# Optimization experiments

Hardware: AMD Instinct MI355X
Metric: run time of the kernel (lower is better)

Reference implementation:

```python
import jax, jax.numpy as jnp
import numpy as np

N_EMBD = 1024
N_HEAD = 16
HEAD_DIM = N_EMBD // N_HEAD


def setup_inputs() -> dict:
    key = jax.random.key(0)
    ks = jax.random.split(key, 6)
    B, T, C = 4, 2048, N_EMBD
    scale = 1.0 / np.sqrt(C)
    x = jax.random.normal(ks[0], (B, T, C), dtype=jnp.float32)
    Wq = jax.random.normal(ks[1], (C, C), dtype=jnp.float32) * scale
    Wk = jax.random.normal(ks[2], (C, C), dtype=jnp.float32) * scale
    Wv = jax.random.normal(ks[3], (C, C), dtype=jnp.float32) * scale
    Wo = jax.random.normal(ks[4], (C, C), dtype=jnp.float32) * scale
    bo = jax.random.normal(ks[5], (C,), dtype=jnp.float32) * 0.01
    return {"x": x, "Wq": Wq, "Wk": Wk, "Wv": Wv, "Wo": Wo, "bo": bo}


def reference(x, Wq, Wk, Wv, Wo, bo):
    B, T, C = x.shape
    H, D = N_HEAD, HEAD_DIM
    # projections (torch Linear: x @ W.T); reshape to [B, H, T, D]
    q = (x @ Wq.T).reshape(B, T, H, D).transpose(0, 2, 1, 3)
    k = (x @ Wk.T).reshape(B, T, H, D).transpose(0, 2, 1, 3)
    v = (x @ Wv.T).reshape(B, T, H, D).transpose(0, 2, 1, 3)
    scores = jnp.einsum("bhqd,bhkd->bhqk", q, k) / np.sqrt(D)
    causal = jnp.tril(jnp.ones((T, T), dtype=bool))  # True = keep
    scores = jnp.where(causal, scores, -jnp.inf)
    attn = jax.nn.softmax(scores, axis=-1)
    # dropout in eval mode = identity
    out = jnp.einsum("bhqk,bhkd->bhqd", attn, v)
    out = out.transpose(0, 2, 1, 3).reshape(B, T, C)
    return out @ Wo.T + bo
```

## Files before the change

### kernel.cpp

```cpp
#include <hip/hip_runtime.h>

typedef __attribute__((ext_vector_type(4))) float floatx4;
typedef __attribute__((ext_vector_type(8))) __bf16 bf16x8;
typedef __attribute__((ext_vector_type(8))) unsigned short ushort8;
typedef __attribute__((ext_vector_type(4))) unsigned short ushort4v;

#define MFMA16(a, b, c) __builtin_amdgcn_mfma_f32_16x16x32_bf16((a), (b), (c), 0, 0, 0)

static __device__ __forceinline__ unsigned short f2bu(float f) {
  unsigned int u = __builtin_bit_cast(unsigned int, f);
  unsigned int r = (u + 0x7fffu + ((u >> 16) & 1u)) >> 16;
  return (unsigned short)r;
}

static __device__ __forceinline__ unsigned int cvtpk(float lo, float hi) {
  unsigned int r;
  asm("v_cvt_pk_bf16_f32 %0, %1, %2" : "=v"(r) : "v"(lo), "v"(hi));
  return r;
}

static __device__ __forceinline__ float fexp2(float x) {
  float r;
  asm("v_exp_f32 %0, %1" : "=v"(r) : "v"(x));
  return r;
}

static __device__ __forceinline__ void gload_lds16(const void* g, void* l) {
  __builtin_amdgcn_global_load_lds((const __attribute__((address_space(1))) void*)g,
                                   (__attribute__((address_space(3))) void*)l, 16, 0, 0);
}

__global__ void cast_all(const float* __restrict__ x,  unsigned short* __restrict__ xb,
                         const float* __restrict__ w0, unsigned short* __restrict__ w0b,
                         const float* __restrict__ w1, unsigned short* __restrict__ w1b,
                         const float* __restrict__ w2, unsigned short* __restrict__ w2b,
                         const float* __restrict__ w3, unsigned short* __restrict__ w3b) {
  int i = blockIdx.x * blockDim.x + threadIdx.x;
  const float* src;
  unsigned short* dst;
  int j;
  if (i < 2097152) {
    src = x; dst = xb; j = i;
  } else {
    j = i - 2097152;
    int wsel = j >> 18;
    j &= 262143;
    src = (wsel == 0) ? w0 : (wsel == 1) ? w1 : (wsel == 2) ? w2 : w3;
    dst = (wsel == 0) ? w0b : (wsel == 1) ? w1b : (wsel == 2) ? w2b : w3b;
  }
  float4 v = reinterpret_cast<const float4*>(src)[j];
  ushort4v o;
  o.x = f2bu(v.x); o.y = f2bu(v.y); o.z = f2bu(v.z); o.w = f2bu(v.w);
  reinterpret_cast<ushort4v*>(dst)[j] = o;
}

static __device__ __forceinline__ void gemm_core(const unsigned short* __restrict__ Ag,
                                                 const unsigned short* __restrict__ Wg,
                                                 int tm0, int tn0,
                                                 unsigned short* As, unsigned short* Bs,
                                                 floatx4 acc[4][4]) {
  const int tid = threadIdx.x;
  const int w = tid >> 6, l = tid & 63;
  const int lg = l >> 4, lq = l & 15;
  const int wr = w >> 1, wc = w & 1;

  const int srow = w * 32 + (l >> 2);
  const int scol = (l & 3) * 8;
  const unsigned short* ga = Ag + (size_t)(tm0 + srow) * 1024 + scol;
  const unsigned short* gb = Wg + (size_t)(tn0 + srow) * 1024 + scol;
  const int ldst0 = w * 1024;
  const int ldst1 = ldst0 + 16 * 32;

#define GSTAGE(bi, kt_)                                   \
  do {                                                    \
    const int ko_ = (kt_) * 32;                           \
    gload_lds16(ga + ko_,              As + (bi) * 4096 + ldst0); \
    gload_lds16(ga + ko_ + 16 * 1024,  As + (bi) * 4096 + ldst1); \
    gload_lds16(gb + ko_,              Bs + (bi) * 4096 + ldst0); \
    gload_lds16(gb + ko_ + 16 * 1024,  Bs + (bi) * 4096 + ldst1); \
  } while (0)

  GSTAGE(0, 0);
  __syncthreads();
  int buf = 0;
  for (int kt = 0; kt < 32; ++kt) {
    if (kt + 1 < 32) GSTAGE(buf ^ 1, kt + 1);
    bf16x8 ar[4], br[4];
#pragma unroll
    for (int i = 0; i < 4; ++i) {
      ar[i] = *(const bf16x8*)(As + buf * 4096 + (wr * 64 + i * 16 + lq) * 32 + lg * 8);
      br[i] = *(const bf16x8*)(Bs + buf * 4096 + (wc * 64 + i * 16 + lq) * 32 + lg * 8);
    }
#pragma unroll
    for (int i = 0; i < 4; ++i)
#pragma unroll
      for (int j = 0; j < 4; ++j)
        acc[i][j] = MFMA16(ar[i], br[j], acc[i][j]);
    __syncthreads();
    buf ^= 1;
  }
#undef GSTAGE
}

__global__ __launch_bounds__(256, 4) void gemm_qkv(const unsigned short* __restrict__ xb,
                                                   const unsigned short* __restrict__ Wqb,
                                                   const unsigned short* __restrict__ Wkb,
                                                   const unsigned short* __restrict__ Wvb,
                                                   unsigned short* __restrict__ Qb,
                                                   unsigned short* __restrict__ Kb,
                                                   unsigned short* __restrict__ Vtb) {
  __shared__ unsigned short As[2 * 128 * 32];
  __shared__ unsigned short Bs[2 * 128 * 32];
  const int tid = threadIdx.x;
  const int w = tid >> 6, l = tid & 63;
  const int lg = l >> 4, lq = l & 15;
  const int wr = w >> 1, wc = w & 1;
  const int tm0 = blockIdx.x * 128;
  const int tn0 = blockIdx.y * 128;
  const int z = blockIdx.z;
  const unsigned short* W = (z == 0) ? Wqb : (z == 1) ? Wkb : Wvb;

  floatx4 acc[4][4];
#pragma unroll
  for (int i = 0; i < 4; ++i)
#pragma unroll
    for (int j = 0; j < 4; ++j) acc[i][j] = (floatx4){0.f, 0.f, 0.f, 0.f};

  gemm_core(xb, W, tm0, tn0, As, Bs, acc);

  const int b = tm0 >> 11;
  const int t0 = tm0 & 2047;

  if (z == 2) {
#pragma unroll
    for (int mi = 0; mi < 4; ++mi)
#pragma unroll
      for (int ni = 0; ni < 4; ++ni) {
        int t = t0 + wr * 64 + mi * 16 + lg * 4;
        int n = tn0 + wc * 64 + ni * 16 + lq;
        int h = n >> 6, d = n & 63;
        ushort4v o;
        o.x = f2bu(acc[mi][ni][0]);
        o.y = f2bu(acc[mi][ni][1]);
        o.z = f2bu(acc[mi][ni][2]);
        o.w = f2bu(acc[mi][ni][3]);
        *(ushort4v*)(Vtb + ((size_t)(b * 16 + h) * 64 + d) * 2048 + t) = o;
      }
  } else {
    float sc = (z == 0) ? 0.125f * 1.44269504f : 1.0f;
    unsigned short* dst = (z == 0) ? Qb : Kb;
#pragma unroll
    for (int mi = 0; mi < 4; ++mi)
#pragma unroll
      for (int ni = 0; ni < 4; ++ni) {
        int n = tn0 + wc * 64 + ni * 16 + lq;
        int h = n >> 6, d = n & 63;
#pragma unroll
        for (int r = 0; r < 4; ++r) {
          int t = t0 + wr * 64 + mi * 16 + lg * 4 + r;
          dst[((size_t)(b * 16 + h) * 2048 + t) * 64 + d] = f2bu(acc[mi][ni][r] * sc);
        }
      }
  }
}

__global__ __launch_bounds__(256) void attn_fwd(const unsigned short* __restrict__ Qb,
                                                const unsigned short* __restrict__ Kb,
                                                const unsigned short* __restrict__ Vtb,
                                                unsigned short* __restrict__ attb) {
  constexpr int T = 2048;
  __shared__ char Ls[32768];
  const int bh = blockIdx.x;
  const int pr = blockIdx.y;
  const int tid = threadIdx.x;
  const int w = tid >> 6, l = tid & 63;
  const int lg = l >> 4, lq = l & 15;

  const char* Kgc = (const char*)(Kb + (size_t)bh * T * 64);
  const char* Vgc = (const char*)(Vtb + (size_t)bh * 64 * T);
  const unsigned short* Qp = Qb + (size_t)bh * T * 64;

  const int scolx = ((tid & 7) << 4) ^ (((tid >> 3) & 7) << 4);
  const int koff = ((tid >> 3) << 7) + scolx;
  const int voff = ((tid >> 3) << 12) + scolx;
  char* Ks = (char*)Ls;
  char* Vs = (char*)Ls + 16384;
  const int kswz = (lq & 7) << 4;
  const int wofs = w * 1024;
  const int b = bh >> 4, h = bh & 15;

  const ushort8 onesu = {0x3F80, 0x3F80, 0x3F80, 0x3F80, 0x3F80, 0x3F80, 0x3F80, 0x3F80};
  const bf16x8 onesf = __builtin_bit_cast(bf16x8, onesu);

#define STAGE(bi, kb_)                                               \
  do {                                                               \
    const char* kg_ = Kgc + (size_t)(kb_) * 128 + koff;              \
    const char* vg_ = Vgc + (size_t)(kb_) * 2 + voff;                \
    gload_lds16(kg_,          Ks + (bi) * 8192 + wofs);              \
    gload_lds16(kg_ + 4096,   Ks + (bi) * 8192 + 4096 + wofs);       \
    gload_lds16(vg_,          Vs + (bi) * 8192 + wofs);              \
    gload_lds16(vg_ + 131072, Vs + (bi) * 8192 + 4096 + wofs);       \
  } while (0)

  for (int pi = 0; pi < 2; ++pi) {
    const int qt = pi ? (31 - pr) : pr;
    const int q0 = qt * 64 + w * 16;
    const int qrow = q0 + lq;

    bf16x8 qf0 = *(const bf16x8*)(Qp + (size_t)qrow * 64 + lg * 8);
    bf16x8 qf1 = *(const bf16x8*)(Qp + (size_t)qrow * 64 + 32 + lg * 8);

    floatx4 acc[4];
#pragma unroll
    for (int dc = 0; dc < 4; ++dc) acc[dc] = (floatx4){0.f, 0.f, 0.f, 0.f};
    floatx4 rsum = (floatx4){0.f, 0.f, 0.f, 0.f};
    float m_run = -1e30f;

    int buf = 0;
    STAGE(0, 0);
    __syncthreads();

    for (int t = 0; t <= qt; ++t) {
      if (t < qt) STAGE(buf ^ 1, (t + 1) * 64);
      const char* Kl = Ks + buf * 8192;
      const char* Vl = Vs + buf * 8192;
      const int kb = t * 64;

      floatx4 s[4];
#pragma unroll
      for (int kc = 0; kc < 4; ++kc) {
        const int rowb = (kc * 16 + lq) * 128;
        bf16x8 kf0 = *(const bf16x8*)(Kl + rowb + ((lg * 16) ^ kswz));
        bf16x8 kf1 = *(const bf16x8*)(Kl + rowb + ((64 + lg * 16) ^ kswz));
        floatx4 tt = (floatx4){0.f, 0.f, 0.f, 0.f};
        tt = MFMA16(kf0, qf0, tt);
        tt = MFMA16(kf1, qf1, tt);
        s[kc] = tt;
      }

      if (t == qt) {
#pragma unroll
        for (int kc = 0; kc < 4; ++kc)
#pragma unroll
          for (int r = 0; r < 4; ++r)
            if (kb + kc * 16 + lg * 4 + r > qrow) s[kc][r] = -1e30f;
      }

      float m0 = fmaxf(fmaxf(s[0][0], s[0][1]), fmaxf(s[0][2], s[0][3]));
      float m1 = fmaxf(fmaxf(s[1][0], s[1][1]), fmaxf(s[1][2], s[1][3]));
      float m2 = fmaxf(fmaxf(s[2][0], s[2][1]), fmaxf(s[2][2], s[2][3]));
      float m3 = fmaxf(fmaxf(s[3][0], s[3][1]), fmaxf(s[3][2], s[3][3]));
      float mt = fmaxf(fmaxf(m0, m1), fmaxf(m2, m3));
      mt = fmaxf(mt, __shfl_xor(mt, 16, 64));
      mt = fmaxf(mt, __shfl_xor(mt, 32, 64));
      if (__any(mt > m_run + 11.f)) {
        float mn = fmaxf(m_run, mt);
        float corr = fexp2(m_run - mn);
#pragma unroll
        for (int dc = 0; dc < 4; ++dc) acc[dc] *= corr;
        rsum *= corr;
        m_run = mn;
      }
      float p[4][4];
#pragma unroll
      for (int kc = 0; kc < 4; ++kc)
#pragma unroll
        for (int r = 0; r < 4; ++r) p[kc][r] = fexp2(s[kc][r] - m_run);

      int4 u0, u1;
      u0.x = cvtpk(p[0][0], p[0][1]); u0.y = cvtpk(p[0][2], p[0][3]);
      u0.z = cvtpk(p[1][0], p[1][1]); u0.w = cvtpk(p[1][2], p[1][3]);
      u1.x = cvtpk(p[2][0], p[2][1]); u1.y = cvtpk(p[2][2], p[2][3]);
      u1.z = cvtpk(p[3][0], p[3][1]); u1.w = cvtpk(p[3][2], p[3][3]);
      bf16x8 pa0 = __builtin_bit_cast(bf16x8, u0);
      bf16x8 pa1 = __builtin_bit_cast(bf16x8, u1);

      rsum = MFMA16(onesf, pa0, rsum);
      rsum = MFMA16(onesf, pa1, rsum);

#pragma unroll
      for (int dc = 0; dc < 4; ++dc) {
        const int rowb = (dc * 16 + lq) * 128;
#pragma unroll
        for (int kk = 0; kk < 2; ++kk) {
          ushort4v v0 = *(const ushort4v*)(Vl + rowb + ((kk * 64 + lg * 8) ^ kswz));
          ushort4v v1 = *(const ushort4v*)(Vl + rowb + ((kk * 64 + lg * 8 + 32) ^ kswz));
          ushort8 vv = __builtin_shufflevector(v0, v1, 0, 1, 2, 3, 4, 5, 6, 7);
          bf16x8 va = __builtin_bit_cast(bf16x8, vv);
          acc[dc] = MFMA16(va, kk ? pa1 : pa0, acc[dc]);
        }
      }
      __syncthreads();
      buf ^= 1;
    }

    float inv = 1.f / rsum[0];
    unsigned short* orow = attb + (size_t)(b * 2048 + qrow) * 1024 + h * 64;
#pragma unroll
    for (int dc = 0; dc < 4; ++dc) {
      ushort4v o;
      o.x = f2bu(acc[dc][0] * inv);
      o.y = f2bu(acc[dc][1] * inv);
      o.z = f2bu(acc[dc][2] * inv);
      o.w = f2bu(acc[dc][3] * inv);
      *(ushort4v*)(orow + 16 * dc + lg * 4) = o;
    }
  }
#undef STAGE
}

__global__ __launch_bounds__(256, 4) void gemm_out(const unsigned short* __restrict__ attb,
                                                   const unsigned short* __restrict__ Wob,
                                                   const float* __restrict__ bo,
                                                   float* __restrict__ out) {
  __shared__ unsigned short As[2 * 128 * 32];
  __shared__ unsigned short Bs[2 * 128 * 32];
  const int tid = threadIdx.x;
  const int w = tid >> 6, l = tid & 63;
  const int lg = l >> 4, lq = l & 15;
  const int wr = w >> 1, wc = w & 1;
  const int tm0 = blockIdx.x * 128;
  const int tn0 = blockIdx.y * 128;

  floatx4 acc[4][4];
#pragma unroll
  for (int i = 0; i < 4; ++i)
#pragma unroll
    for (int j = 0; j < 4; ++j) acc[i][j] = (floatx4){0.f, 0.f, 0.f, 0.f};

  gemm_core(attb, Wob, tm0, tn0, As, Bs, acc);

#pragma unroll
  for (int mi = 0; mi < 4; ++mi)
#pragma unroll
    for (int ni = 0; ni < 4; ++ni) {
      int row = tm0 + wr * 64 + mi * 16 + lg * 4;
      int col = tn0 + wc * 64 + ni * 16 + lq;
      float bias = bo[col];
#pragma unroll
      for (int r = 0; r < 4; ++r)
        out[(size_t)(row + r) * 1024 + col] = acc[mi][ni][r] + bias;
    }
}

extern "C" void kernel_launch(void* const* d_in, const int* in_sizes, int n_in,
                              void* d_out, int out_size, void* d_ws, size_t ws_size,
                              hipStream_t stream) {
  const float* x  = (const float*)d_in[0];
  const float* Wq = (const float*)d_in[1];
  const float* Wk = (const float*)d_in[2];
  const float* Wv = (const float*)d_in[3];
  const float* Wo = (const float*)d_in[4];
  const float* bo = (const float*)d_in[5];
  float* out = (float*)d_out;

  unsigned short* ws = (unsigned short*)d_ws;
  unsigned short* xb  = ws;
  unsigned short* Wqb = ws + 8388608;
  unsigned short* Wkb = ws + 9437184;
  unsigned short* Wvb = ws + 10485760;
  unsigned short* Wob = ws + 11534336;
  unsigned short* Qb  = ws + 12582912;
  unsigned short* Kb  = ws + 20971520;
  unsigned short* Vtb = ws + 29360128;
  unsigned short* attb= ws + 37748736;

  cast_all<<<12288, 256, 0, stream>>>(x, xb, Wq, Wqb, Wk, Wkb, Wv, Wvb, Wo, Wob);

  gemm_qkv<<<dim3(64, 8, 3), 256, 0, stream>>>(xb, Wqb, Wkb, Wvb, Qb, Kb, Vtb);
  attn_fwd<<<dim3(64, 16), 256, 0, stream>>>(Qb, Kb, Vtb, attb);
  gemm_out<<<dim3(64, 8), 256, 0, stream>>>(attb, Wob, bo, out);
}
```

Baseline: 257.2 us.

## Enlarge attention query tile to 256 rows per block for K/V reuse

Each attention block now processes 256 query rows (64 per wave, four 16-row sub-tiles) instead of two paired 64-row tiles. Each K/V tile staged in LDS is reused across four times as many queries, which cuts global and LDS traffic per FLOP. Blocks are dispatched longest-first through a permutation table, and launch bounds now request 2 blocks per CU. The costs are much higher register pressure (16 accumulator vectors plus the per-subtile score tiles), only 512 blocks, and some waves idling on diagonal tiles where their rows are fully masked.

```diff
diff --git a/kernel.cpp b/kernel.cpp
--- a/kernel.cpp
+++ b/kernel.cpp
@@ -164,14 +164,14 @@
   }
 }
 
-__global__ __launch_bounds__(256) void attn_fwd(const unsigned short* __restrict__ Qb,
-                                                const unsigned short* __restrict__ Kb,
-                                                const unsigned short* __restrict__ Vtb,
-                                                unsigned short* __restrict__ attb) {
+__global__ __launch_bounds__(256, 2) void attn_fwd(const unsigned short* __restrict__ Qb,
+                                                   const unsigned short* __restrict__ Kb,
+                                                   const unsigned short* __restrict__ Vtb,
+                                                   unsigned short* __restrict__ attb) {
   constexpr int T = 2048;
   __shared__ char Ls[32768];
   const int bh = blockIdx.x;
-  const int pr = blockIdx.y;
+  const int qt = (0x34251607u >> (blockIdx.y * 4)) & 7;
   const int tid = threadIdx.x;
   const int w = tid >> 6, l = tid & 63;
   const int lg = l >> 4, lq = l & 15;
@@ -202,81 +202,99 @@
     gload_lds16(vg_ + 131072, Vs + (bi) * 8192 + 4096 + wofs);       \
   } while (0)
 
-  for (int pi = 0; pi < 2; ++pi) {
-    const int qt = pi ? (31 - pr) : pr;
-    const int q0 = qt * 64 + w * 16;
-    const int qrow = q0 + lq;
-
-    bf16x8 qf0 = *(const bf16x8*)(Qp + (size_t)qrow * 64 + lg * 8);
-    bf16x8 qf1 = *(const bf16x8*)(Qp + (size_t)qrow * 64 + 32 + lg * 8);
-
-    floatx4 acc[4];
-#pragma unroll
-    for (int dc = 0; dc < 4; ++dc) acc[dc] = (floatx4){0.f, 0.f, 0.f, 0.f};
-    floatx4 rsum = (floatx4){0.f, 0.f, 0.f, 0.f};
-    float m_run = -1e30f;
-
-    int buf = 0;
-    STAGE(0, 0);
-    __syncthreads();
-
-    for (int t = 0; t <= qt; ++t) {
-      if (t < qt) STAGE(buf ^ 1, (t + 1) * 64);
+  const int q0 = qt * 256 + w * 64;
+
+  bf16x8 qf[4][2];
+#pragma unroll
+  for (int qh = 0; qh < 4; ++qh) {
+    qf[qh][0] = *(const bf16x8*)(Qp + (size_t)(q0 + qh * 16 + lq) * 64 + lg * 8);
+    qf[qh][1] = *(const bf16x8*)(Qp + (size_t)(q0 + qh * 16 + lq) * 64 + 32 + lg * 8);
+  }
+
+  floatx4 acc[4][4];
+#pragma unroll
+  for (int qh = 0; qh < 4; ++qh)
+#pragma unroll
+    for (int dc = 0; dc < 4; ++dc) acc[qh][dc] = (floatx4){0.f, 0.f, 0.f, 0.f};
+  floatx4 rsum[4];
+#pragma unroll
+  for (int qh = 0; qh < 4; ++qh) rsum[qh] = (floatx4){0.f, 0.f, 0.f, 0.f};
+  float m_run[4] = {-1e30f, -1e30f, -1e30f, -1e30f};
+
+  const int nt = 4 * qt + 4;
+  int buf = 0;
+  STAGE(0, 0);
+  __syncthreads();
+
+  for (int t = 0; t < nt; ++t) {
+    if (t + 1 < nt) STAGE(buf ^ 1, (t + 1) * 64);
+    const int kb = t * 64;
+    if (kb <= q0 + 63) {
       const char* Kl = Ks + buf * 8192;
       const char* Vl = Vs + buf * 8192;
-      const int kb = t * 64;
-
-      floatx4 s[4];
+
+      floatx4 s[4][4];
 #pragma unroll
       for (int kc = 0; kc < 4; ++kc) {
         const int rowb = (kc * 16 + lq) * 128;
         bf16x8 kf0 = *(const bf16x8*)(Kl + rowb + ((lg * 16) ^ kswz));
         bf16x8 kf1 = *(const bf16x8*)(Kl + rowb + ((64 + lg * 16) ^ kswz));
-        floatx4 tt = (floatx4){0.f, 0.f, 0.f, 0.f};
-        tt = MFMA16(kf0, qf0, tt);
-        tt = MFMA16(kf1, qf1, tt);
-        s[kc] = tt;
-      }
-
-      if (t == qt) {
+#pragma unroll
+        for (int qh = 0; qh < 4; ++qh) {
+          floatx4 tt = (floatx4){0.f, 0.f, 0.f, 0.f};
+          tt = MFMA16(kf0, qf[qh][0], tt);
+          tt = MFMA16(kf1, qf[qh][1], tt);
+          s[qh][kc] = tt;
+        }
+      }
+
+      if (kb + 63 > q0) {
+#pragma unroll
+        for (int qh = 0; qh < 4; ++qh) {
+          const int qrow = q0 + qh * 16 + lq;
+#pragma unroll
+          for (int kc = 0; kc < 4; ++kc)
+#pragma unroll
+            for (int r = 0; r < 4; ++r)
+              if (kb + kc * 16 + lg * 4 + r > qrow) s[qh][kc][r] = -1e30f;
+        }
+      }
+
+      bf16x8 pa[4][2];
+#pragma unroll
+      for (int qh = 0; qh < 4; ++qh) {
+        float m0 = fmaxf(fmaxf(s[qh][0][0], s[qh][0][1]), fmaxf(s[qh][0][2], s[qh][0][3]));
+        float m1 = fmaxf(fmaxf(s[qh][1][0], s[qh][1][1]), fmaxf(s[qh][1][2], s[qh][1][3]));
+        float m2 = fmaxf(fmaxf(s[qh][2][0], s[qh][2][1]), fmaxf(s[qh][2][2], s[qh][2][3]));
+        float m3 = fmaxf(fmaxf(s[qh][3][0], s[qh][3][1]), fmaxf(s[qh][3][2], s[qh][3][3]));
+        float mt = fmaxf(fmaxf(m0, m1), fmaxf(m2, m3));
+        mt = fmaxf(mt, __shfl_xor(mt, 16, 64));
+        mt = fmaxf(mt, __shfl_xor(mt, 32, 64));
+        if (__any(mt > m_run[qh] + 11.f)) {
+          float mn = fmaxf(m_run[qh], mt);
+          float corr = fexp2(m_run[qh] - mn);
+#pragma unroll
+          for (int dc = 0; dc < 4; ++dc) acc[qh][dc] *= corr;
+          rsum[qh] *= corr;
+          m_run[qh] = mn;
+        }
+        float p[4][4];
 #pragma unroll
         for (int kc = 0; kc < 4; ++kc)
 #pragma unroll
-          for (int r = 0; r < 4; ++r)
-            if (kb + kc * 16 + lg * 4 + r > qrow) s[kc][r] = -1e30f;
-      }
-
-      float m0 = fmaxf(fmaxf(s[0][0], s[0][1]), fmaxf(s[0][2], s[0][3]));
-      float m1 = fmaxf(fmaxf(s[1][0], s[1][1]), fmaxf(s[1][2], s[1][3]));
-      float m2 = fmaxf(fmaxf(s[2][0], s[2][1]), fmaxf(s[2][2], s[2][3]));
-      float m3 = fmaxf(fmaxf(s[3][0], s[3][1]), fmaxf(s[3][2], s[3][3]));
-      float mt = fmaxf(fmaxf(m0, m1), fmaxf(m2, m3));
-      mt = fmaxf(mt, __shfl_xor(mt, 16, 64));
-      mt = fmaxf(mt, __shfl_xor(mt, 32, 64));
-      if (__any(mt > m_run + 11.f)) {
-        float mn = fmaxf(m_run, mt);
-        float corr = fexp2(m_run - mn);
-#pragma unroll
-        for (int dc = 0; dc < 4; ++dc) acc[dc] *= corr;
-        rsum *= corr;
-        m_run = mn;
-      }
-      float p[4][4];
-#pragma unroll
-      for (int kc = 0; kc < 4; ++kc)
-#pragma unroll
-        for (int r = 0; r < 4; ++r) p[kc][r] = fexp2(s[kc][r] - m_run);
-
-      int4 u0, u1;
-      u0.x = cvtpk(p[0][0], p[0][1]); u0.y = cvtpk(p[0][2], p[0][3]);
-      u0.z = cvtpk(p[1][0], p[1][1]); u0.w = cvtpk(p[1][2], p[1][3]);
-      u1.x = cvtpk(p[2][0], p[2][1]); u1.y = cvtpk(p[2][2], p[2][3]);
-      u1.z = cvtpk(p[3][0], p[3][1]); u1.w = cvtpk(p[3][2], p[3][3]);
-      bf16x8 pa0 = __builtin_bit_cast(bf16x8, u0);
-      bf16x8 pa1 = __builtin_bit_cast(bf16x8, u1);
-
-      rsum = MFMA16(onesf, pa0, rsum);
-      rsum = MFMA16(onesf, pa1, rsum);
+          for (int r = 0; r < 4; ++r) p[kc][r] = fexp2(s[qh][kc][r] - m_run[qh]);
+
+        int4 u0, u1;
+        u0.x = cvtpk(p[0][0], p[0][1]); u0.y = cvtpk(p[0][2], p[0][3]);
+        u0.z = cvtpk(p[1][0], p[1][1]); u0.w = cvtpk(p[1][2], p[1][3]);
+        u1.x = cvtpk(p[2][0], p[2][1]); u1.y = cvtpk(p[2][2], p[2][3]);
+        u1.z = cvtpk(p[3][0], p[3][1]); u1.w = cvtpk(p[3][2], p[3][3]);
+        pa[qh][0] = __builtin_bit_cast(bf16x8, u0);
+        pa[qh][1] = __builtin_bit_cast(bf16x8, u1);
+
+        rsum[qh] = MFMA16(onesf, pa[qh][0], rsum[qh]);
+        rsum[qh] = MFMA16(onesf, pa[qh][1], rsum[qh]);
+      }
 
 #pragma unroll
       for (int dc = 0; dc < 4; ++dc) {
@@ -287,22 +305,27 @@
           ushort4v v1 = *(const ushort4v*)(Vl + rowb + ((kk * 64 + lg * 8 + 32) ^ kswz));
           ushort8 vv = __builtin_shufflevector(v0, v1, 0, 1, 2, 3, 4, 5, 6, 7);
           bf16x8 va = __builtin_bit_cast(bf16x8, vv);
-          acc[dc] = MFMA16(va, kk ? pa1 : pa0, acc[dc]);
-        }
-      }
-      __syncthreads();
-      buf ^= 1;
+#pragma unroll
+          for (int qh = 0; qh < 4; ++qh)
+            acc[qh][dc] = MFMA16(va, pa[qh][kk], acc[qh][dc]);
+        }
+      }
     }
-
-    float inv = 1.f / rsum[0];
-    unsigned short* orow = attb + (size_t)(b * 2048 + qrow) * 1024 + h * 64;
+    __syncthreads();
+    buf ^= 1;
+  }
+
+#pragma unroll
+  for (int qh = 0; qh < 4; ++qh) {
+    float inv = 1.f / rsum[qh][0];
+    unsigned short* orow = attb + (size_t)(b * 2048 + q0 + qh * 16 + lq) * 1024 + h * 64;
 #pragma unroll
     for (int dc = 0; dc < 4; ++dc) {
       ushort4v o;
-      o.x = f2bu(acc[dc][0] * inv);
-      o.y = f2bu(acc[dc][1] * inv);
-      o.z = f2bu(acc[dc][2] * inv);
-      o.w = f2bu(acc[dc][3] * inv);
+      o.x = f2bu(acc[qh][dc][0] * inv);
+      o.y = f2bu(acc[qh][dc][1] * inv);
+      o.z = f2bu(acc[qh][dc][2] * inv);
+      o.w = f2bu(acc[qh][dc][3] * inv);
       *(ushort4v*)(orow + 16 * dc + lg * 4) = o;
     }
   }
@@ -368,6 +391,6 @@
   cast_all<<<12288, 256, 0, stream>>>(x, xb, Wq, Wqb, Wk, Wkb, Wv, Wvb, Wo, Wob);
 
   gemm_qkv<<<dim3(64, 8, 3), 256, 0, stream>>>(xb, Wqb, Wkb, Wvb, Qb, Kb, Vtb);
-  attn_fwd<<<dim3(64, 16), 256, 0, stream>>>(Qb, Kb, Vtb, attb);
+  attn_fwd<<<dim3(64, 8), 256, 0, stream>>>(Qb, Kb, Vtb, attb);
   gemm_out<<<dim3(64, 8), 256, 0, stream>>>(attb, Wob, bo, out);
 }
```

Measured after the change: 261.6 us. Within noise of the previous version (+1.7%).
